# Performance work log

Measured on AMD Instinct MI355X. Metric: run time of the kernel, lower is better.

## Reference

```python
import jax, jax.numpy as jnp
import numpy as np

B, S, K, N, GROUP = 4, 8, 4096, 11008, 128
NUM_GROUPS = K // GROUP  # 32


def setup_inputs() -> dict:
    key = jax.random.key(0)
    k1, k2, k3 = jax.random.split(key, 3)
    x = jax.random.normal(k1, (B, S, K), dtype=jnp.float16)
    # packed int4 weights: each byte holds two nibbles (low nibble = even k, high = odd k)
    weight_packed = jax.random.randint(k2, (N, K // 2), 0, 256, dtype=jnp.int32)
    # scales: abs(randn)*0.1 in fp16, as in the torch module
    scales = (jnp.abs(jax.random.normal(k3, (N, NUM_GROUPS), dtype=jnp.float16)) * jnp.float16(0.1))
    return {"x": x, "weight_packed": weight_packed, "scales": scales}


def _dequant(weight_packed, scales, Kd):
    # unpack: low nibble -> even index k, high nibble -> odd index k+1
    n = weight_packed.shape[0]
    low = weight_packed & 0xF
    high = (weight_packed >> 4) & 0xF
    w = jnp.stack([low, high], axis=-1).reshape(n, Kd)  # [N, K] int in [0,16)
    g = Kd // scales.shape[1]
    # group-wise dequant: scale * (w - 8), scale applied in fp32 (matches fp32-accum kernel)
    wq = (w.astype(jnp.float32) - 8.0).reshape(n, scales.shape[1], g)
    wdeq = wq * scales.astype(jnp.float32)[:, :, None]
    return wdeq.reshape(n, Kd)  # [N, K] fp32


def reference(x, weight_packed, scales):
    b, s, kd = x.shape
    wdeq = _dequant(weight_packed, scales, kd)           # [N, K]
    x2 = x.reshape(-1, kd).astype(jnp.float32)           # [M, K], fp32 accumulation
    out = jnp.einsum('mk,nk->mn', x2, wdeq)              # [M, N]
    return out.astype(jnp.float16).reshape(b, s, -1)
```

## Files before the change

kernel.cpp:

```cpp
#include <hip/hip_runtime.h>

#define M 32
#define N 11008
#define K 4096
#define NGROUPS 32
#define KSPLIT 4
#define KRANGE (K / KSPLIT)
#define BK 256
#define NCHUNK (KRANGE / BK)
#define MN (M * N)

typedef _Float16 half8 __attribute__((ext_vector_type(8)));
typedef _Float16 half4 __attribute__((ext_vector_type(4)));
typedef float floatx4 __attribute__((ext_vector_type(4)));

#define WPAIR 260

__device__ inline void gll16(const void* g, void* l) {
    __builtin_amdgcn_global_load_lds(
        (const __attribute__((address_space(1))) unsigned int*)g,
        (__attribute__((address_space(3))) unsigned int*)l, 16, 0, 0);
}

__global__ __launch_bounds__(512) void xcvt_kernel(
    const float* __restrict__ x, _Float16* __restrict__ xf)
{
    int i = (blockIdx.x * 512 + threadIdx.x) * 4;
    float4 v = *(const float4*)(x + i);
    half4 h;
    h[0] = (_Float16)v.x; h[1] = (_Float16)v.y;
    h[2] = (_Float16)v.z; h[3] = (_Float16)v.w;
    *(half4*)(xf + i) = h;
}

__global__ __launch_bounds__(256, 8) void int4_gemm_kernel(
    const _Float16* __restrict__ xf,
    const int* __restrict__ wp,
    const float* __restrict__ scales,
    float* __restrict__ out)
{
    __shared__ int wsh[8 * WPAIR];

    const int t    = threadIdx.x;
    const int lane = t & 63;
    const int w    = t >> 6;
    const int n0   = blockIdx.x * 16;
    const int ks   = blockIdx.y;
    const int row  = lane & 15;
    const int quad = lane >> 4;
    const int nw   = n0 + row;

    const half8 c1032 = (half8)(_Float16)1032.0f;
    floatx4 acc0 = {0.f, 0.f, 0.f, 0.f};
    floatx4 acc1 = {0.f, 0.f, 0.f, 0.f};

    for (int c = 0; c < NCHUNK; ++c) {
        const int k0 = ks * KRANGE + c * BK;

        #pragma unroll
        for (int i = 0; i < 2; ++i) {
            int p = w * 2 + i;
            int r = 2 * p + (lane >> 5);
            const int* g = wp + (long)(n0 + r) * (K / 2) + (k0 >> 1) + (lane & 31) * 4;
            gll16(g, &wsh[p * WPAIR]);
        }
        __syncthreads();

        const int kw = k0 + w * 64;
        half8 a[2][2];
        #pragma unroll
        for (int kk = 0; kk < 2; ++kk)
            #pragma unroll
            for (int i = 0; i < 2; ++i)
                a[kk][i] = *(const half8*)(xf + (i * 16 + row) * K + kw + kk * 32 + quad * 8);

        const float s = scales[nw * NGROUPS + (k0 >> 7) + (w >> 1)];

        floatx4 t0 = {0.f, 0.f, 0.f, 0.f};
        floatx4 t1 = {0.f, 0.f, 0.f, 0.f};
        #pragma unroll
        for (int kk = 0; kk < 2; ++kk) {
            int4 wv = *(const int4*)&wsh[(row >> 1) * WPAIR + (row & 1) * 128
                                         + w * 32 + kk * 16 + quad * 4];
            uint4 uw;
            {
                unsigned int b;
                b = (unsigned int)wv.x; uw.x = ((b | (b << 12)) & 0x000F000Fu) | 0x64006400u;
                b = (unsigned int)wv.y; uw.y = ((b | (b << 12)) & 0x000F000Fu) | 0x64006400u;
                b = (unsigned int)wv.z; uw.z = ((b | (b << 12)) & 0x000F000Fu) | 0x64006400u;
                b = (unsigned int)wv.w; uw.w = ((b | (b << 12)) & 0x000F000Fu) | 0x64006400u;
            }
            half8 bfrag = __builtin_bit_cast(half8, uw) - c1032;
            t0 = __builtin_amdgcn_mfma_f32_16x16x32_f16(a[kk][0], bfrag, t0, 0, 0, 0);
            t1 = __builtin_amdgcn_mfma_f32_16x16x32_f16(a[kk][1], bfrag, t1, 0, 0, 0);
        }
        #pragma unroll
        for (int r = 0; r < 4; ++r) {
            acc0[r] += s * t0[r];
            acc1[r] += s * t1[r];
        }
        __syncthreads();
    }

    float* red = (float*)wsh;
    #pragma unroll
    for (int r = 0; r < 4; ++r) {
        red[w * 512 + (quad * 4 + r) * 16 + row]      = acc0[r];
        red[w * 512 + (quad * 4 + r + 16) * 16 + row] = acc1[r];
    }
    __syncthreads();
    #pragma unroll
    for (int i = 0; i < 2; ++i) {
        int o = t + 256 * i;
        float sum = red[o] + red[512 + o] + red[1024 + o] + red[1536 + o];
        int m = o >> 4;
        int n = o & 15;
        atomicAdd(&out[m * N + n0 + n], sum);
    }
}

extern "C" void kernel_launch(void* const* d_in, const int* in_sizes, int n_in,
                              void* d_out, int out_size, void* d_ws, size_t ws_size,
                              hipStream_t stream) {
    const float* x      = (const float*)d_in[0];
    const int* wp       = (const int*)d_in[1];
    const float* scales = (const float*)d_in[2];
    float* out          = (float*)d_out;
    _Float16* xf16      = (_Float16*)d_ws;

    hipMemsetAsync(out, 0, (size_t)MN * sizeof(float), stream);
    xcvt_kernel<<<dim3((M * K) / (512 * 4)), 512, 0, stream>>>(x, xf16);
    int4_gemm_kernel<<<dim3(N / 16, KSPLIT), 256, 0, stream>>>(xf16, wp, scales, out);
}
```

Baseline: 149.8 us.

## Stage activations and weights through LDS with register loads instead of direct global-to-LDS

Replaces the global_load_lds weight staging with ordinary vector global loads into registers, then stores them to a padded LDS tile. The activation tile is now loaded cooperatively into padded shared memory too, rather than each wave reading its MFMA A fragments straight from global memory. The aim is coalesced activation reads with fewer bank conflicts. The cost is more LDS per block and extra LDS store/read traffic, and the occupancy hint of 8 blocks was removed from launch bounds.

```diff
diff --git a/kernel.cpp b/kernel.cpp
--- a/kernel.cpp
+++ b/kernel.cpp
@@ -14,13 +14,8 @@
 typedef _Float16 half4 __attribute__((ext_vector_type(4)));
 typedef float floatx4 __attribute__((ext_vector_type(4)));
 
-#define WPAIR 260
-
-__device__ inline void gll16(const void* g, void* l) {
-    __builtin_amdgcn_global_load_lds(
-        (const __attribute__((address_space(1))) unsigned int*)g,
-        (__attribute__((address_space(3))) unsigned int*)l, 16, 0, 0);
-}
+#define WROW 132
+#define XROW 264
 
 __global__ __launch_bounds__(512) void xcvt_kernel(
     const float* __restrict__ x, _Float16* __restrict__ xf)
@@ -33,13 +28,14 @@
     *(half4*)(xf + i) = h;
 }
 
-__global__ __launch_bounds__(256, 8) void int4_gemm_kernel(
+__global__ __launch_bounds__(256) void int4_gemm_kernel(
     const _Float16* __restrict__ xf,
     const int* __restrict__ wp,
     const float* __restrict__ scales,
     float* __restrict__ out)
 {
-    __shared__ int wsh[8 * WPAIR];
+    __shared__ __align__(16) int wsh[16 * WROW];
+    __shared__ __align__(16) _Float16 xs[32 * XROW];
 
     const int t    = threadIdx.x;
     const int lane = t & 63;
@@ -49,6 +45,8 @@
     const int row  = lane & 15;
     const int quad = lane >> 4;
     const int nw   = n0 + row;
+    const int half32 = lane >> 5;
+    const int l32  = lane & 31;
 
     const half8 c1032 = (half8)(_Float16)1032.0f;
     floatx4 acc0 = {0.f, 0.f, 0.f, 0.f};
@@ -57,31 +55,37 @@
     for (int c = 0; c < NCHUNK; ++c) {
         const int k0 = ks * KRANGE + c * BK;
 
+        int4 wv0, wv1;
+        {
+            int r0 = w * 4 + half32;
+            int r1 = r0 + 2;
+            wv0 = *(const int4*)(wp + (long)(n0 + r0) * (K / 2) + (k0 >> 1) + l32 * 4);
+            wv1 = *(const int4*)(wp + (long)(n0 + r1) * (K / 2) + (k0 >> 1) + l32 * 4);
+        }
+        uint4 xv[4];
         #pragma unroll
-        for (int i = 0; i < 2; ++i) {
-            int p = w * 2 + i;
-            int r = 2 * p + (lane >> 5);
-            const int* g = wp + (long)(n0 + r) * (K / 2) + (k0 >> 1) + (lane & 31) * 4;
-            gll16(g, &wsh[p * WPAIR]);
+        for (int i = 0; i < 4; ++i) {
+            int m = w * 8 + i * 2 + half32;
+            xv[i] = *(const uint4*)(xf + m * K + k0 + l32 * 8);
+        }
+        {
+            int r0 = w * 4 + half32, r1 = r0 + 2;
+            *(int4*)&wsh[r0 * WROW + l32 * 4] = wv0;
+            *(int4*)&wsh[r1 * WROW + l32 * 4] = wv1;
+        }
+        #pragma unroll
+        for (int i = 0; i < 4; ++i) {
+            int m = w * 8 + i * 2 + half32;
+            *(uint4*)&xs[m * XROW + l32 * 8] = xv[i];
         }
         __syncthreads();
 
-        const int kw = k0 + w * 64;
-        half8 a[2][2];
-        #pragma unroll
-        for (int kk = 0; kk < 2; ++kk)
-            #pragma unroll
-            for (int i = 0; i < 2; ++i)
-                a[kk][i] = *(const half8*)(xf + (i * 16 + row) * K + kw + kk * 32 + quad * 8);
-
         const float s = scales[nw * NGROUPS + (k0 >> 7) + (w >> 1)];
-
         floatx4 t0 = {0.f, 0.f, 0.f, 0.f};
         floatx4 t1 = {0.f, 0.f, 0.f, 0.f};
         #pragma unroll
         for (int kk = 0; kk < 2; ++kk) {
-            int4 wv = *(const int4*)&wsh[(row >> 1) * WPAIR + (row & 1) * 128
-                                         + w * 32 + kk * 16 + quad * 4];
+            int4 wv = *(const int4*)&wsh[row * WROW + w * 32 + kk * 16 + quad * 4];
             uint4 uw;
             {
                 unsigned int b;
@@ -91,8 +95,10 @@
                 b = (unsigned int)wv.w; uw.w = ((b | (b << 12)) & 0x000F000Fu) | 0x64006400u;
             }
             half8 bfrag = __builtin_bit_cast(half8, uw) - c1032;
-            t0 = __builtin_amdgcn_mfma_f32_16x16x32_f16(a[kk][0], bfrag, t0, 0, 0, 0);
-            t1 = __builtin_amdgcn_mfma_f32_16x16x32_f16(a[kk][1], bfrag, t1, 0, 0, 0);
+            half8 a0 = *(const half8*)&xs[row * XROW + w * 64 + kk * 32 + quad * 8];
+            half8 a1 = *(const half8*)&xs[(row + 16) * XROW + w * 64 + kk * 32 + quad * 8];
+            t0 = __builtin_amdgcn_mfma_f32_16x16x32_f16(a0, bfrag, t0, 0, 0, 0);
+            t1 = __builtin_amdgcn_mfma_f32_16x16x32_f16(a1, bfrag, t1, 0, 0, 0);
         }
         #pragma unroll
         for (int r = 0; r < 4; ++r) {
@@ -102,7 +108,7 @@
         __syncthreads();
     }
 
-    float* red = (float*)wsh;
+    float* red = (float*)xs;
     #pragma unroll
     for (int r = 0; r < 4; ++r) {
         red[w * 512 + (quad * 4 + r) * 16 + row]      = acc0[r];
```

After: 149.2 us. Within noise of the previous version (-0.4%).
